# Kernel optimization log

Measured on AMD Instinct MI355X. Metric: run time of the kernel, lower is better.

The kernel has to match this reference:

```python
import jax, jax.numpy as jnp
import numpy as np

ATTRACTION_W = 1.0
REPULSION_W = 1.0
MARGIN = 0.3  # hardcoded local `margin = 0.3` in the torch forward


def setup_inputs() -> dict:
    key = jax.random.key(0)
    k1, k2, k3 = jax.random.split(key, 3)
    B, N, D, K = 16, 65536, 32, 512
    beta = jax.random.normal(k1, (B, N, 1), dtype=jnp.float32)
    embed = jax.random.normal(k2, (B, N, D), dtype=jnp.float32)
    # instance id per hit: -1 = background, 0..K-1 = instances
    sid = jax.random.randint(k3, (B, N), -1, K).astype(jnp.int32)
    # first K hits are the condensation points, one per instance
    sid = sid.at[:, :K].set(jnp.arange(K, dtype=jnp.int32)[None, :])
    is_cp = jnp.zeros((B, N), dtype=jnp.int32).at[:, :K].set(1)
    return {"beta": beta, "embed": embed, "slice_id": sid, "is_cp": is_cp, "num_instances": K}


def _per_batch(beta_b, emb_b, sid, iscp, K):
    # beta_b: [N], emb_b: [N, D], sid/iscp: [N]
    N = sid.shape[0]
    cp = iscp == 1
    valid = sid >= 0
    noncp = valid & ~cp  # non-cp signal hits
    pos = cp.sum().astype(jnp.float32)
    neg = jnp.float32(N) - pos  # noncp + background
    pos_w = jax.lax.stop_gradient(neg / (pos + 1e-6))
    w = jnp.where(cp, pos_w, jnp.where(noncp, 1.0, 2.0))
    # weighted BCE-with-logits, reduction='mean'
    x = beta_b
    y = cp.astype(jnp.float32)
    bce = jnp.maximum(x, 0.0) - x * y + jnp.log1p(jnp.exp(-jnp.abs(x)))
    beta_ce = (w * bce).mean()

    # segment id: valid hits -> sid, background -> dummy segment K (dropped)
    seg = jnp.where(valid, sid, K)
    counts = jax.ops.segment_sum(valid.astype(jnp.float32), seg, num_segments=K + 1)[:K]
    inst_exists = counts > 0  # the `unique()` set

    # first cp hit index per instance (sentinel N if instance has no cp)
    idxs = jnp.arange(N)
    first_cp = jax.ops.segment_min(jnp.where(cp & valid, idxs, N), seg, num_segments=K + 1)[:K]
    has_cp = first_cp < N
    safe_cp = jnp.minimum(first_cp, N - 1)
    cp_emb = emb_b[safe_cp]  # [K, D]
    cp_beta = beta_b[safe_cp]  # [K]

    # attraction: sum over instances (with a cp) of mean ||e_hit - e_cp||^2
    sid_c = jnp.clip(sid, 0, K - 1)
    d2 = ((emb_b - cp_emb[sid_c]) ** 2).sum(-1)  # [N]
    d2 = jnp.where(valid, d2, 0.0)
    seg_d2 = jax.ops.segment_sum(d2, seg, num_segments=K + 1)[:K]
    attr = (jnp.where(has_cp & inst_exists, seg_d2 / jnp.maximum(counts, 1.0), 0.0).sum()
            * ATTRACTION_W)

    # ranking: instances with exactly 1 cp and >0 noncp hits
    cp_count = jax.ops.segment_sum((cp & valid).astype(jnp.float32), seg, num_segments=K + 1)[:K]
    ncp_count = jax.ops.segment_sum(noncp.astype(jnp.float32), seg, num_segments=K + 1)[:K]
    r = jax.nn.relu(beta_b + MARGIN - cp_beta[sid_c])
    r = jnp.where(noncp, r, 0.0)
    seg_r = jax.ops.segment_sum(r, seg, num_segments=K + 1)[:K]
    qual = (cp_count == 1.0) & (ncp_count > 0)
    n_unique = inst_exists.sum().astype(jnp.float32)
    ranking = (jnp.where(qual, seg_r / jnp.maximum(ncp_count, 1.0), 0.0).sum()
               / jnp.maximum(n_unique, 1.0))

    beta_loss = beta_ce + 2.0 * ranking

    # repulsion over all cp hits; data has exactly one cp per instance so the
    # cp set equals cp_emb (K points), matching torch's emb_b[cp_idx]
    diff = cp_emb[:, None, :] - cp_emb[None, :, :]  # [K, K, D]
    rep = jnp.exp(-(diff ** 2).sum(-1)).mean() * REPULSION_W

    return beta_loss + attr + rep, beta_loss, attr, rep


def reference(beta, embed, slice_id, is_cp, num_instances):
    K = int(num_instances)
    beta2 = beta[..., 0]  # squeeze(-1)
    loss_b, bl, al, rl = jax.vmap(lambda b, e, s, c: _per_batch(b, e, s, c, K))(
        beta2, embed, slice_id, is_cp)
    return loss_b.mean(), bl.mean(), al.mean(), rl.mean()
```

## Files before the change

kernel.cpp:

```cpp
#include <hip/hip_runtime.h>
#include <math.h>

#define N_HITS 65536
#define K_INST 512
#define MARGIN 0.3f
#define THREADS 512
#define BPB    64
#define HITS_PB (N_HITS / BPB)

__device__ __forceinline__ unsigned short f2bf(float f) {
    unsigned u = __float_as_uint(f);
    return (unsigned short)((u + 0x7FFFu + ((u >> 16) & 1u)) >> 16);
}
__device__ __forceinline__ float bf2f(unsigned short h) {
    return __uint_as_float(((unsigned)h) << 16);
}

__global__ __launch_bounds__(256) void k_scan(
    const int* __restrict__ sid, const int* __restrict__ iscp,
    int* first_cp, int* pos_cnt) {
    int b = blockIdx.y;
    size_t bo = (size_t)b * N_HITS;
    int i = blockIdx.x * 256 + threadIdx.x;
    int stride = gridDim.x * 256;
    for (; i < N_HITS; i += stride) {
        int c = iscp[bo + i];
        if (c == 1) {
            atomicAdd(&pos_cnt[b], 1);
            int s = sid[bo + i];
            if (s >= 0) atomicMin(&first_cp[b * K_INST + s], i);
        }
    }
}

__global__ __launch_bounds__(256) void k_gather(
    const float* __restrict__ beta, const float4* __restrict__ embed4,
    const int* __restrict__ first_cp,
    float* cp_beta, float4* cp_emb4, int B) {
    int g = blockIdx.x * 256 + threadIdx.x;
    int total = B * K_INST * 8;
    if (g >= total) return;
    int row = g >> 3, sub = g & 7;
    int b = row / K_INST;
    int fc = first_cp[row];
    int safe = min(fc, N_HITS - 1);
    float4 e = embed4[((size_t)b * N_HITS + safe) * 8 + sub];
    cp_emb4[(size_t)row * 8 + sub] = e;
    if (sub == 0) cp_beta[row] = beta[b * N_HITS + safe];
}

__global__ __launch_bounds__(THREADS, 4) void k_main(
    const float*  __restrict__ beta,
    const float4* __restrict__ embed4,
    const int*    __restrict__ sid_g, const int* __restrict__ iscp_g,
    const float4* __restrict__ cp_emb4, const float* __restrict__ cp_beta,
    int* pc_cnt, float* pc_d2, float* pc_r,
    int* cnt_packed, float* seg_d2, float* seg_r,
    float* s_cp, float* s_ncp, float* s_bg, int use_part) {
    __shared__ float4 l_cp[K_INST * 8];
    __shared__ float l_d2[K_INST];
    __shared__ int   l_cnt[K_INST];
    __shared__ float l_r[K_INST];
    __shared__ float l_cb[K_INST];
    __shared__ short st_s[HITS_PB];
    __shared__ float l_red[24];

    int b = blockIdx.y, tid = threadIdx.x;
    size_t bo = (size_t)b * N_HITS;
    int base = blockIdx.x * HITS_PB;

    {
        const float4* cpt = cp_emb4 + (size_t)b * K_INST * 8;
        for (int idx = tid; idx < K_INST * 8; idx += THREADS) l_cp[idx] = cpt[idx];
    }
    for (int k = tid; k < K_INST; k += THREADS) {
        l_cnt[k] = 0; l_r[k] = 0.f; l_d2[k] = 0.f;
        l_cb[k] = cp_beta[b * K_INST + k];
    }
    __syncthreads();

    float a_cp = 0.f, a_ncp = 0.f, a_bg = 0.f;
    {
        int s0 = sid_g[bo + base + tid];
        int s1 = sid_g[bo + base + THREADS + tid];
        int c0 = iscp_g[bo + base + tid];
        int c1 = iscp_g[bo + base + THREADS + tid];
        float x0 = beta[bo + base + tid];
        float x1 = beta[bo + base + THREADS + tid];
        st_s[tid]           = (short)s0;
        st_s[THREADS + tid] = (short)s1;
#pragma unroll
        for (int h = 0; h < 2; ++h) {
            int s = h ? s1 : s0;
            int c = h ? c1 : c0;
            float x = h ? x1 : x0;
            bool cp = (c == 1), valid = (s >= 0), noncp = valid && !cp;
            float t = __expf(-fabsf(x));
            float bce = fmaxf(x, 0.f) - (cp ? x : 0.f) + __logf(1.f + t);
            if (cp) a_cp += bce; else if (noncp) a_ncp += bce; else a_bg += bce;
            if (valid) {
                atomicAdd(&l_cnt[s], cp ? (1 << 20) : 1);
                if (noncp) {
                    float r = x + MARGIN - l_cb[s];
                    if (r > 0.f) atomicAdd(&l_r[s], r);
                }
            }
        }
    }
    __syncthreads();

    {
        int sub = tid & 7, hgrp = tid >> 3;
        constexpr int NIT = HITS_PB / 64;
        size_t ebase = (bo + base + hgrp) * 8 + sub;
        short sarr[NIT];
#pragma unroll
        for (int it = 0; it < NIT; ++it) sarr[it] = st_s[it * 64 + hgrp];
#pragma unroll
        for (int half = 0; half < 2; ++half) {
            float4 pe[8];
            float4 pc[8];
#pragma unroll
            for (int j = 0; j < 8; ++j) {
                pe[j] = embed4[ebase + (size_t)(half * 8 + j) * 512];
            }
#pragma unroll
            for (int j = 0; j < 8; ++j) {
                pc[j] = l_cp[max((int)sarr[half * 8 + j], 0) * 8 + sub];
            }
#pragma unroll
            for (int j = 0; j < 8; ++j) {
                int s = sarr[half * 8 + j];
                float dx = pe[j].x - pc[j].x, dy = pe[j].y - pc[j].y;
                float dz = pe[j].z - pc[j].z, dw = pe[j].w - pc[j].w;
                float q = dx * dx + dy * dy + dz * dz + dw * dw;
                q += __shfl_xor(q, 1);
                q += __shfl_xor(q, 2);
                q += __shfl_xor(q, 4);
                if (sub == 0 && s >= 0) atomicAdd(&l_d2[s], q);
            }
        }
    }

    for (int o = 32; o > 0; o >>= 1) {
        a_cp  += __shfl_down(a_cp, o);
        a_ncp += __shfl_down(a_ncp, o);
        a_bg  += __shfl_down(a_bg, o);
    }
    int wave = tid >> 6;
    if ((tid & 63) == 0) { l_red[wave] = a_cp; l_red[8 + wave] = a_ncp; l_red[16 + wave] = a_bg; }
    __syncthreads();
    if (tid == 0) {
        float t0 = 0.f, t1 = 0.f, t2 = 0.f;
        for (int w = 0; w < 8; ++w) { t0 += l_red[w]; t1 += l_red[8 + w]; t2 += l_red[16 + w]; }
        atomicAdd(&s_cp[b],  t0);
        atomicAdd(&s_ncp[b], t1);
        atomicAdd(&s_bg[b],  t2);
    }
    if (use_part) {
        size_t po = ((size_t)b * BPB + blockIdx.x) * K_INST;
        for (int k = tid; k < K_INST; k += THREADS) {
            pc_cnt[po + k] = l_cnt[k];
            pc_d2[po + k]  = l_d2[k];
            pc_r[po + k]   = l_r[k];
        }
    } else {
        for (int k = tid; k < K_INST; k += THREADS) {
            int cv = l_cnt[k]; if (cv) atomicAdd(&cnt_packed[b * K_INST + k], cv);
            float dv = l_d2[k]; if (dv != 0.f) atomicAdd(&seg_d2[b * K_INST + k], dv);
            float rv = l_r[k]; if (rv != 0.f) atomicAdd(&seg_r[b * K_INST + k], rv);
        }
    }
}

__global__ __launch_bounds__(256) void k_reduce(
    const int* __restrict__ pc_cnt, const float* __restrict__ pc_d2,
    const float* __restrict__ pc_r,
    int* cnt_packed, float* seg_d2, float* seg_r) {
    __shared__ int   rc[4][64];
    __shared__ float rd[4][64];
    __shared__ float rr[4][64];
    int kl = threadIdx.x & 63, p4 = threadIdx.x >> 6;
    int bin = blockIdx.x * 64 + kl;
    int b = bin / K_INST;
    size_t basep = ((size_t)b * BPB) * K_INST + (bin % K_INST);
    int cs = 0; float ds = 0.f, rs = 0.f;
    for (int p = p4 * (BPB / 4); p < (p4 + 1) * (BPB / 4); ++p) {
        cs += pc_cnt[basep + (size_t)p * K_INST];
        ds += pc_d2[basep + (size_t)p * K_INST];
        rs += pc_r[basep + (size_t)p * K_INST];
    }
    rc[p4][kl] = cs; rd[p4][kl] = ds; rr[p4][kl] = rs;
    __syncthreads();
    if (p4 == 0) {
        cnt_packed[bin] = rc[0][kl] + rc[1][kl] + rc[2][kl] + rc[3][kl];
        seg_d2[bin]     = rd[0][kl] + rd[1][kl] + rd[2][kl] + rd[3][kl];
        seg_r[bin]      = rr[0][kl] + rr[1][kl] + rr[2][kl] + rr[3][kl];
    }
}

__global__ __launch_bounds__(512) void k_tail(
    const float4* __restrict__ cp_emb4,
    const int* __restrict__ cnt_packed, const float* __restrict__ seg_d2,
    const float* __restrict__ seg_r, const int* __restrict__ first_cp,
    const int* __restrict__ pos_cnt, const float* __restrict__ s_cp,
    const float* __restrict__ s_ncp, const float* __restrict__ s_bg,
    float* attr_b, float* rank_b, float* nuniq_b, float* rep_b,
    int* ctr, float* out, int B) {
    int tid = threadIdx.x;
    int nrep = B * 16;

    if ((int)blockIdx.x < nrep) {
        __shared__ float4 tile[32 * 8];
        __shared__ float red[8];
        int b = blockIdx.x >> 4, t2 = blockIdx.x & 15;
        const float4* base = cp_emb4 + (size_t)b * K_INST * 8;
        float4 r0[8];
#pragma unroll
        for (int cc = 0; cc < 8; ++cc) r0[cc] = base[(size_t)tid * 8 + cc];
        if (tid < 256) tile[tid] = base[(size_t)t2 * 256 + tid];
        __syncthreads();
        float acc = 0.f;
        for (int j = 0; j < 32; ++j) {
            float d2 = 0.f;
#pragma unroll
            for (int cc = 0; cc < 8; ++cc) {
                float4 ev = tile[j * 8 + cc];
                float ax = r0[cc].x - ev.x, ay = r0[cc].y - ev.y;
                float az = r0[cc].z - ev.z, aw = r0[cc].w - ev.w;
                d2 += ax * ax + ay * ay + az * az + aw * aw;
            }
            acc += __expf(-d2);
        }
        for (int o = 32; o > 0; o >>= 1) acc += __shfl_down(acc, o);
        if ((tid & 63) == 0) red[tid >> 6] = acc;
        __syncthreads();
        if (tid == 0) {
            float t = 0.f;
            for (int w = 0; w < 8; ++w) t += red[w];
            atomicAdd(&rep_b[b], t);
        }
    } else {
        __shared__ float red2[3][8];
        int b = blockIdx.x - nrep, k = tid;
        int v = cnt_packed[b * K_INST + k];
        int ncp = v & 0xFFFFF, cpc = v >> 20;
        int counts = ncp + cpc;
        int fc = first_cp[b * K_INST + k];
        bool has_cp = fc < N_HITS, exists = counts > 0;
        float segd = seg_d2[b * K_INST + k];
        float attr = (has_cp && exists) ? segd / fmaxf((float)counts, 1.f) : 0.f;
        float rank = (cpc == 1 && ncp > 0) ? seg_r[b * K_INST + k] / fmaxf((float)ncp, 1.f) : 0.f;
        float uq = exists ? 1.f : 0.f;
        for (int o = 32; o > 0; o >>= 1) {
            attr += __shfl_down(attr, o);
            rank += __shfl_down(rank, o);
            uq   += __shfl_down(uq, o);
        }
        if ((k & 63) == 0) { red2[0][k >> 6] = attr; red2[1][k >> 6] = rank; red2[2][k >> 6] = uq; }
        __syncthreads();
        if (k == 0) {
            float a = 0.f, r = 0.f, u = 0.f;
            for (int w = 0; w < 8; ++w) { a += red2[0][w]; r += red2[1][w]; u += red2[2][w]; }
            attr_b[b] = a; rank_b[b] = r; nuniq_b[b] = u;
        }
    }

    __shared__ int is_last;
    __syncthreads();
    if (tid == 0) {
        __threadfence();
        int v = atomicAdd(ctr, 1);
        is_last = (v == (int)gridDim.x - 1);
    }
    __syncthreads();
    if (is_last) {
        __threadfence();
        if (tid < 64) {
            int b = tid;
            float loss = 0.f, bl = 0.f, at = 0.f, rp = 0.f;
            if (b < B) {
                float pos = (float)pos_cnt[b];
                float pw = ((float)N_HITS - pos) / (pos + 1e-6f);
                float bce = (pw * s_cp[b] + s_ncp[b] + 2.f * s_bg[b]) / (float)N_HITS;
                float rank = rank_b[b] / fmaxf(nuniq_b[b], 1.f);
                bl = bce + 2.f * rank;
                at = attr_b[b];
                rp = rep_b[b] / (float)(K_INST * K_INST);
                loss = bl + at + rp;
            }
            for (int o = 32; o > 0; o >>= 1) {
                loss += __shfl_down(loss, o);
                bl   += __shfl_down(bl, o);
                at   += __shfl_down(at, o);
                rp   += __shfl_down(rp, o);
            }
            if (tid == 0) {
                float inv = 1.f / (float)B;
                out[0] = loss * inv;
                out[1] = bl * inv;
                out[2] = at * inv;
                out[3] = rp * inv;
            }
        }
    }
}

extern "C" void kernel_launch(void* const* d_in, const int* in_sizes, int n_in,
                              void* d_out, int out_size, void* d_ws, size_t ws_size,
                              hipStream_t stream) {
    const float*  beta   = (const float*)d_in[0];
    const float*  embed  = (const float*)d_in[1];
    const int*    sid    = (const int*)d_in[2];
    const int*    iscp   = (const int*)d_in[3];
    float* out = (float*)d_out;

    int BN = in_sizes[0];
    int B  = BN / N_HITS;
    int BK = B * K_INST;

    char* ws = (char*)d_ws;
    int*   cnt_packed = (int*)ws;
    float* seg_d2     = (float*)(ws + 4 * (size_t)BK);
    float* seg_r      = (float*)(ws + 8 * (size_t)BK);
    float* scal       = (float*)(ws + 12 * (size_t)BK);
    int*   pos_cnt  = (int*)scal;
    float* s_cp     = scal + 1 * B;
    float* s_ncp    = scal + 2 * B;
    float* s_bg     = scal + 3 * B;
    float* attr_b   = scal + 4 * B;
    float* rank_b   = scal + 5 * B;
    float* nuniq_b  = scal + 6 * B;
    float* rep_b    = scal + 7 * B;
    int*   ctr      = (int*)(scal + 8 * B);
    size_t zbytes = 12 * (size_t)BK + 32 * (size_t)B + 16;
    int*     first_cp = (int*)(ws + zbytes);
    float*   cp_beta  = (float*)(ws + zbytes + 4 * (size_t)BK);
    float4*  cp_emb4  = (float4*)(ws + zbytes + 8 * (size_t)BK);
    char*    partbase = ws + zbytes + 8 * (size_t)BK + 128 * (size_t)BK;
    size_t   psz      = (size_t)B * BPB * K_INST * 4;
    int*     pc_cnt   = (int*)partbase;
    float*   pc_d2    = (float*)(partbase + psz);
    float*   pc_r     = (float*)(partbase + 2 * psz);
    size_t   need     = (size_t)(partbase - ws) + 3 * psz;
    int use_part = (ws_size >= need) ? 1 : 0;

    hipMemsetAsync(ws, 0, zbytes, stream);
    hipMemsetAsync(first_cp, 0x7F, 4 * (size_t)BK, stream);

    k_scan<<<dim3(32, B), 256, 0, stream>>>(sid, iscp, first_cp, pos_cnt);

    k_gather<<<(BK * 8 + 255) / 256, 256, 0, stream>>>(beta, (const float4*)embed,
                                                       first_cp, cp_beta, cp_emb4, B);

    k_main<<<dim3(BPB, B), THREADS, 0, stream>>>(beta, (const float4*)embed, sid, iscp,
                                                 (const float4*)cp_emb4, cp_beta,
                                                 pc_cnt, pc_d2, pc_r,
                                                 cnt_packed, seg_d2, seg_r,
                                                 s_cp, s_ncp, s_bg, use_part);

    if (use_part)
        k_reduce<<<BK / 64, 256, 0, stream>>>(pc_cnt, pc_d2, pc_r,
                                              cnt_packed, seg_d2, seg_r);

    k_tail<<<B * 16 + B, 512, 0, stream>>>((const float4*)cp_emb4,
                                           cnt_packed, seg_d2, seg_r,
                                           first_cp, pos_cnt, s_cp, s_ncp, s_bg,
                                           attr_b, rank_b, nuniq_b, rep_b,
                                           ctr, out, B);
}
```

Measured before the change: 246.3 us.

## Compute per-hit distance in one thread with XOR-swizzled LDS centroid table

Restructures the main kernel so that each thread owns whole hits and reads all 8 float4s of its embedding row, rather than spreading a hit across 8 lanes and combining partial sums with shuffles. The centroid table in LDS is XOR-swizzled to reduce bank conflicts on the per-thread row reads. Blocks per batch drop from 64 to 32, so each thread handles 4 hits, and the intermediate shared sid staging plus one barrier are removed. The trade-off is strided per-thread global loads of 128-byte rows, which coalesce less well across a wave, plus higher register pressure and fewer blocks.

After: 245.1 us. Within noise of the previous version (-0.5%).

```diff
diff --git a/kernel.cpp b/kernel.cpp
--- a/kernel.cpp
+++ b/kernel.cpp
@@ -5,16 +5,8 @@
 #define K_INST 512
 #define MARGIN 0.3f
 #define THREADS 512
-#define BPB    64
+#define BPB    32
 #define HITS_PB (N_HITS / BPB)
-
-__device__ __forceinline__ unsigned short f2bf(float f) {
-    unsigned u = __float_as_uint(f);
-    return (unsigned short)((u + 0x7FFFu + ((u >> 16) & 1u)) >> 16);
-}
-__device__ __forceinline__ float bf2f(unsigned short h) {
-    return __uint_as_float(((unsigned)h) << 16);
-}
 
 __global__ __launch_bounds__(256) void k_scan(
     const int* __restrict__ sid, const int* __restrict__ iscp,
@@ -58,11 +50,10 @@
     int* cnt_packed, float* seg_d2, float* seg_r,
     float* s_cp, float* s_ncp, float* s_bg, int use_part) {
     __shared__ float4 l_cp[K_INST * 8];
-    __shared__ float l_d2[K_INST];
+    __shared__ float l_cb[K_INST];
     __shared__ int   l_cnt[K_INST];
     __shared__ float l_r[K_INST];
-    __shared__ float l_cb[K_INST];
-    __shared__ short st_s[HITS_PB];
+    __shared__ float l_d2[K_INST];
     __shared__ float l_red[24];
 
     int b = blockIdx.y, tid = threadIdx.x;
@@ -71,7 +62,10 @@
 
     {
         const float4* cpt = cp_emb4 + (size_t)b * K_INST * 8;
-        for (int idx = tid; idx < K_INST * 8; idx += THREADS) l_cp[idx] = cpt[idx];
+        for (int idx = tid; idx < K_INST * 8; idx += THREADS) {
+            int k = idx >> 3, j = idx & 7;
+            l_cp[(k << 3) | (j ^ (k & 7))] = cpt[idx];
+        }
     }
     for (int k = tid; k < K_INST; k += THREADS) {
         l_cnt[k] = 0; l_r[k] = 0.f; l_d2[k] = 0.f;
@@ -80,64 +74,53 @@
     __syncthreads();
 
     float a_cp = 0.f, a_ncp = 0.f, a_bg = 0.f;
-    {
-        int s0 = sid_g[bo + base + tid];
-        int s1 = sid_g[bo + base + THREADS + tid];
-        int c0 = iscp_g[bo + base + tid];
-        int c1 = iscp_g[bo + base + THREADS + tid];
-        float x0 = beta[bo + base + tid];
-        float x1 = beta[bo + base + THREADS + tid];
-        st_s[tid]           = (short)s0;
-        st_s[THREADS + tid] = (short)s1;
-#pragma unroll
-        for (int h = 0; h < 2; ++h) {
-            int s = h ? s1 : s0;
-            int c = h ? c1 : c0;
-            float x = h ? x1 : x0;
-            bool cp = (c == 1), valid = (s >= 0), noncp = valid && !cp;
+
+    int sv[4], cv[4];
+    float xv[4];
+#pragma unroll
+    for (int i = 0; i < 4; ++i) {
+        size_t h = bo + base + i * THREADS + tid;
+        sv[i] = sid_g[h];
+        cv[i] = iscp_g[h];
+        xv[i] = beta[h];
+    }
+
+#pragma unroll
+    for (int pp = 0; pp < 2; ++pp) {
+        float4 e[2][8];
+#pragma unroll
+        for (int i = 0; i < 2; ++i) {
+            size_t ebase = (bo + base + (pp * 2 + i) * THREADS + tid) * 8;
+#pragma unroll
+            for (int j = 0; j < 8; ++j) e[i][j] = embed4[ebase + j];
+        }
+#pragma unroll
+        for (int i = 0; i < 2; ++i) {
+            int hi = pp * 2 + i;
+            int s = sv[hi];
+            bool cp = (cv[hi] == 1), valid = (s >= 0), noncp = valid && !cp;
+            float x = xv[hi];
             float t = __expf(-fabsf(x));
             float bce = fmaxf(x, 0.f) - (cp ? x : 0.f) + __logf(1.f + t);
             if (cp) a_cp += bce; else if (noncp) a_ncp += bce; else a_bg += bce;
+
+            int sc = max(s, 0);
+            int rowb = sc << 3, sw = sc & 7;
+            float d2 = 0.f;
+#pragma unroll
+            for (int j = 0; j < 8; ++j) {
+                float4 cc = l_cp[rowb | (j ^ sw)];
+                float dx = e[i][j].x - cc.x, dy = e[i][j].y - cc.y;
+                float dz = e[i][j].z - cc.z, dw = e[i][j].w - cc.w;
+                d2 += dx * dx + dy * dy + dz * dz + dw * dw;
+            }
             if (valid) {
                 atomicAdd(&l_cnt[s], cp ? (1 << 20) : 1);
+                atomicAdd(&l_d2[s], d2);
                 if (noncp) {
                     float r = x + MARGIN - l_cb[s];
                     if (r > 0.f) atomicAdd(&l_r[s], r);
                 }
-            }
-        }
-    }
-    __syncthreads();
-
-    {
-        int sub = tid & 7, hgrp = tid >> 3;
-        constexpr int NIT = HITS_PB / 64;
-        size_t ebase = (bo + base + hgrp) * 8 + sub;
-        short sarr[NIT];
-#pragma unroll
-        for (int it = 0; it < NIT; ++it) sarr[it] = st_s[it * 64 + hgrp];
-#pragma unroll
-        for (int half = 0; half < 2; ++half) {
-            float4 pe[8];
-            float4 pc[8];
-#pragma unroll
-            for (int j = 0; j < 8; ++j) {
-                pe[j] = embed4[ebase + (size_t)(half * 8 + j) * 512];
-            }
-#pragma unroll
-            for (int j = 0; j < 8; ++j) {
-                pc[j] = l_cp[max((int)sarr[half * 8 + j], 0) * 8 + sub];
-            }
-#pragma unroll
-            for (int j = 0; j < 8; ++j) {
-                int s = sarr[half * 8 + j];
-                float dx = pe[j].x - pc[j].x, dy = pe[j].y - pc[j].y;
-                float dz = pe[j].z - pc[j].z, dw = pe[j].w - pc[j].w;
-                float q = dx * dx + dy * dy + dz * dz + dw * dw;
-                q += __shfl_xor(q, 1);
-                q += __shfl_xor(q, 2);
-                q += __shfl_xor(q, 4);
-                if (sub == 0 && s >= 0) atomicAdd(&l_d2[s], q);
             }
         }
     }
@@ -166,7 +149,7 @@
         }
     } else {
         for (int k = tid; k < K_INST; k += THREADS) {
-            int cv = l_cnt[k]; if (cv) atomicAdd(&cnt_packed[b * K_INST + k], cv);
+            int cc = l_cnt[k]; if (cc) atomicAdd(&cnt_packed[b * K_INST + k], cc);
             float dv = l_d2[k]; if (dv != 0.f) atomicAdd(&seg_d2[b * K_INST + k], dv);
             float rv = l_r[k]; if (rv != 0.f) atomicAdd(&seg_r[b * K_INST + k], rv);
         }
```
